# Kernel tuning notes

Hardware: AMD Instinct MI355X
Metric: run time of the kernel (lower is better)

## Reference

```python
import jax, jax.numpy as jnp
import numpy as np

B, M, L, D = 64, 128, 20, 1024


def setup_inputs() -> dict:
    key = jax.random.key(0)
    ks = jax.random.split(key, 16)
    s = 0.05  # weight scale to keep LSTM gates out of saturation
    rn = lambda k, shape: jax.random.normal(k, shape, jnp.float32) * s
    return {
        'encoder_out': jax.random.normal(ks[0], (B, M + 1, D), jnp.float32),
        'obj_seq': jax.random.randint(ks[1], (B, L), 0, M),
        'att_mask': jnp.ones((B, M + 1), jnp.int32),
        'bos_w': rn(ks[2], (1, D)),
        'eos_w': rn(ks[3], (1, D)),
        'Wp': rn(ks[4], (D, D)), 'bp': jnp.zeros((D,), jnp.float32),
        'Wih1': rn(ks[5], (4 * D, 3 * D)), 'Whh1': rn(ks[6], (4 * D, D)),
        'bih1': jnp.zeros((4 * D,), jnp.float32), 'bhh1': jnp.zeros((4 * D,), jnp.float32),
        'Wih2': rn(ks[7], (4 * D, 2 * D)), 'Whh2': rn(ks[8], (4 * D, D)),
        'bih2': jnp.zeros((4 * D,), jnp.float32), 'bhh2': jnp.zeros((4 * D,), jnp.float32),
        'Wah': rn(ks[9], (D, D)), 'bah': jnp.zeros((D,), jnp.float32),
        'wa': rn(ks[10], (D,)), 'ba': jnp.zeros((1,), jnp.float32),
        'Wae': rn(ks[11], (D, D)), 'bae': jnp.zeros((D,), jnp.float32),
        'Woe': rn(ks[12], (D, D)), 'boe': jnp.zeros((D,), jnp.float32),
    }


def _lstm_cell(x, h, c, Wih, Whh, bih, bhh):
    # torch LSTMCell gate order: i, f, g, o
    g = x @ Wih.T + bih + h @ Whh.T + bhh
    i, f, gg, o = jnp.split(g, 4, axis=-1)
    c_new = jax.nn.sigmoid(f) * c + jax.nn.sigmoid(i) * jnp.tanh(gg)
    h_new = jax.nn.sigmoid(o) * jnp.tanh(c_new)
    return h_new, c_new


def _forward(encoder_out, obj_seq, att_mask, bos_w, eos_w, Wp, bp,
             Wih1, Whh1, bih1, bhh1, Wih2, Whh2, bih2, bhh2,
             Wah, bah, wa, ba, Wae, bae, Woe, boe):
    b, _, d = encoder_out.shape
    gv = encoder_out[:, 0, :]                      # [B, D]
    att_feats = encoder_out[:, 1:, :]              # [B, M, D]
    idx = jnp.broadcast_to(obj_seq[:, :, None], obj_seq.shape + (d,)).astype(jnp.int32)
    obj_feat = jnp.take_along_axis(att_feats, idx, axis=1)          # [B, L, D]
    bos = jnp.broadcast_to(bos_w, (b, 1, d))
    obj_feat = jnp.concatenate([bos, obj_feat], axis=1)             # [B, L+1, D]
    p_att = att_feats @ Wp.T + bp                  # [B, M, D]
    amask = att_mask[:, 1:]                        # [B, M]

    def attend(h1):
        dot = jnp.tanh(p_att + (h1 @ Wah.T + bah)[:, None, :])      # [B, M, D]
        score = dot @ wa + ba[0]                                    # [B, M]
        score = jnp.where(amask == 0, -1e9, score)
        alpha = jax.nn.softmax(score, axis=-1)
        return jnp.einsum('bm,bmd->bd', alpha, att_feats)

    def step(carry, x_t):
        h1, c1, h2, c2 = carry
        inp1 = jnp.concatenate([h2, gv, x_t], axis=-1)              # [B, 3D]
        h1, c1 = _lstm_cell(inp1, h1, c1, Wih1, Whh1, bih1, bhh1)
        att = attend(h1)
        inp2 = jnp.concatenate([att, h1], axis=-1)                  # [B, 2D]
        h2, c2 = _lstm_cell(inp2, h2, c2, Wih2, Whh2, bih2, bhh2)
        return (h1, c1, h2, c2), h2

    z = jnp.zeros((b, d), encoder_out.dtype)
    _, outs = jax.lax.scan(step, (z, z, z, z), jnp.swapaxes(obj_feat, 0, 1))
    outputs = jnp.swapaxes(outs, 0, 1)             # [B, L+1, D]

    # NCE branch (cfg.LOSSES.NCE.STOP_GRAD = True)
    nce_att = jax.lax.stop_gradient(att_feats)
    afe = nce_att @ Wae.T + bae
    eos = jnp.broadcast_to(eos_w, (b, 1, d))
    afe = jnp.concatenate([eos, afe], axis=1)      # [B, M+1, D]
    ofe = outputs @ Woe.T + boe                    # [B, L+1, D]
    nce_logit = jnp.einsum('bld,bmd->blm', ofe, afe)  # [B, L+1, M+1]
    return outputs, nce_logit


def reference(encoder_out, obj_seq, att_mask, bos_w, eos_w, Wp, bp,
              Wih1, Whh1, bih1, bhh1, Wih2, Whh2, bih2, bhh2,
              Wah, bah, wa, ba, Wae, bae, Woe, boe):
    return _forward(encoder_out, obj_seq, att_mask, bos_w, eos_w, Wp, bp,
                    Wih1, Whh1, bih1, bhh1, Wih2, Whh2, bih2, bhh2,
                    Wah, bah, wa, ba, Wae, bae, Woe, boe)
```

## Files before the change

kernel.cpp:

```cpp
#include <hip/hip_runtime.h>
#include <cmath>

typedef unsigned short u16;
typedef __attribute__((ext_vector_type(8))) short short8;
typedef __attribute__((ext_vector_type(4))) float floatx4;
typedef __attribute__((address_space(3))) unsigned int lds_u32;
typedef const __attribute__((address_space(1))) unsigned int glob_u32;

__device__ __forceinline__ u16 f2bf(float f) {
    unsigned u = __float_as_uint(f);
    unsigned r = u + 0x7fffu + ((u >> 16) & 1u);
    return (u16)(r >> 16);
}
__device__ __forceinline__ float bf2f(u16 h) { return __uint_as_float(((unsigned)h) << 16); }
__device__ __forceinline__ void split2(float x, u16& hi, u16& lo) {
    hi = f2bf(x);
    lo = f2bf(x - bf2f(hi));
}
__device__ __forceinline__ float sigm(float x) {
    x = fminf(fmaxf(x, -30.f), 30.f);
    return 1.0f / (1.0f + __expf(-x));
}
__device__ __forceinline__ float ftanh(float x) {
    x = fminf(fmaxf(x, -15.f), 15.f);
    float e = __expf(2.f * x);
    return (e - 1.f) / (e + 1.f);
}
__device__ __forceinline__ void gload16(const void* g, void* l) {
    __builtin_amdgcn_global_load_lds((glob_u32*)g, (lds_u32*)l, 16, 0, 0);
}

__global__ __launch_bounds__(256) void k_cvt(const float* __restrict__ s, u16* __restrict__ d, int n4) {
    int i = blockIdx.x * 256 + threadIdx.x;
    int stride = gridDim.x * 256;
    for (; i < n4; i += stride) {
        float4 v = ((const float4*)s)[i];
        ushort4 o;
        o.x = f2bf(v.x); o.y = f2bf(v.y); o.z = f2bf(v.z); o.w = f2bf(v.w);
        ((ushort4*)d)[i] = o;
    }
}

__global__ __launch_bounds__(256) void k_cvt_att(const float* __restrict__ enc, u16* __restrict__ dst) {
    int m = blockIdx.x, b = blockIdx.y, tid = threadIdx.x;
    const float* src = enc + ((size_t)b * 129 + 1 + m) * 1024;
    float4 v = *(const float4*)(src + tid * 4);
    ushort4 o;
    o.x = f2bf(v.x); o.y = f2bf(v.y); o.z = f2bf(v.z); o.w = f2bf(v.w);
    *(ushort4*)(dst + ((size_t)b * 128 + m) * 1024 + tid * 4) = o;
}

__global__ __launch_bounds__(256) void k_splitp(const float* __restrict__ s, u16* __restrict__ hi,
                                                u16* __restrict__ lo, int n4) {
    int i = blockIdx.x * 256 + threadIdx.x;
    int stride = gridDim.x * 256;
    for (; i < n4; i += stride) {
        float4 v = ((const float4*)s)[i];
        ushort4 h, l;
        split2(v.x, h.x, l.x); split2(v.y, h.y, l.y);
        split2(v.z, h.z, l.z); split2(v.w, h.w, l.w);
        ((ushort4*)hi)[i] = h;
        ((ushort4*)lo)[i] = l;
    }
}

__global__ __launch_bounds__(256) void k_build_w1cat(const float* __restrict__ Wih1, const float* __restrict__ Whh1,
                                                     u16* __restrict__ dh, u16* __restrict__ dl) {
    int row = blockIdx.x;
    int c = threadIdx.x * 8;
    const float* src = (c < 1024) ? (Wih1 + (size_t)row * 3072 + c) : (Whh1 + (size_t)row * 1024 + (c - 1024));
    short8 h, l;
#pragma unroll
    for (int j = 0; j < 8; ++j) { u16 hh, ll; split2(src[j], hh, ll); h[j] = (short)hh; l[j] = (short)ll; }
    *(short8*)(dh + (size_t)row * 2048 + c) = h;
    *(short8*)(dl + (size_t)row * 2048 + c) = l;
}

__global__ __launch_bounds__(384) void k_build_wcat2(const float* __restrict__ Wih2, const float* __restrict__ Whh2,
                                                     u16* __restrict__ dh, u16* __restrict__ dl) {
    int row = blockIdx.x;
    int c = threadIdx.x * 8;
    const float* src = (c < 2048) ? (Wih2 + (size_t)row * 2048 + c) : (Whh2 + (size_t)row * 1024 + (c - 2048));
    short8 h, l;
#pragma unroll
    for (int j = 0; j < 8; ++j) { u16 hh, ll; split2(src[j], hh, ll); h[j] = (short)hh; l[j] = (short)ll; }
    *(short8*)(dh + (size_t)row * 3072 + c) = h;
    *(short8*)(dl + (size_t)row * 3072 + c) = l;
}

__global__ __launch_bounds__(256) void k_build_wx1(const float* __restrict__ Wih1, u16* __restrict__ dh,
                                                   u16* __restrict__ dl) {
    int row = blockIdx.x;
    int c = threadIdx.x * 8;
    const float* src = Wih1 + (size_t)row * 3072 + 1024 + c;
    short8 h, l;
#pragma unroll
    for (int j = 0; j < 8; ++j) { u16 hh, ll; split2(src[j], hh, ll); h[j] = (short)hh; l[j] = (short)ll; }
    *(short8*)(dh + (size_t)row * 2048 + c) = h;
    *(short8*)(dl + (size_t)row * 2048 + c) = l;
}

__global__ __launch_bounds__(256) void k_build_xaug(const float* __restrict__ enc, const int* __restrict__ obj,
                                                    const float* __restrict__ bos_w, u16* __restrict__ dh,
                                                    u16* __restrict__ dl) {
    int b = blockIdx.x, t = blockIdx.y, tid = threadIdx.x;
    const float* gv = enc + (size_t)b * 129 * 1024;
    const float* xr;
    if (t == 0) xr = bos_w;
    else {
        int idx = obj[b * 20 + (t - 1)];
        idx = min(max(idx, 0), 127);
        xr = enc + ((size_t)b * 129 + 1 + idx) * 1024;
    }
    size_t rowoff = ((size_t)b * 21 + t) * 2048;
    float4 v0 = *(const float4*)(gv + tid * 4);
    float4 v1 = *(const float4*)(xr + tid * 4);
    ushort4 h0, l0, h1, l1;
    split2(v0.x, h0.x, l0.x); split2(v0.y, h0.y, l0.y); split2(v0.z, h0.z, l0.z); split2(v0.w, h0.w, l0.w);
    split2(v1.x, h1.x, l1.x); split2(v1.y, h1.y, l1.y); split2(v1.z, h1.z, l1.z); split2(v1.w, h1.w, l1.w);
    *(ushort4*)(dh + rowoff + tid * 4) = h0;
    *(ushort4*)(dl + rowoff + tid * 4) = l0;
    *(ushort4*)(dh + rowoff + 1024 + tid * 4) = h1;
    *(ushort4*)(dl + rowoff + 1024 + tid * 4) = l1;
}

template <int APASS, int BPASS, int AREMAP, bool BF16OUT>
__global__ __launch_bounds__(256)
void k_gemm3(const u16* __restrict__ Ah, const u16* __restrict__ Al, int lda,
             const u16* __restrict__ Wh, const u16* __restrict__ Wl, int ldw,
             const float* __restrict__ b1, const float* __restrict__ b2,
             void* __restrict__ Cout, int ldc, int Mrows, int K) {
    constexpr int NP = APASS + BPASS;
    __shared__ char lds[2][NP][8192];
    const int tid = threadIdx.x;
    const int lane = tid & 63;
    const int lr = lane & 15, lk = lane >> 4;
    const int m0 = blockIdx.y * 128, n0 = blockIdx.x * 128;
    const int wid = tid >> 6;
    const int wr = wid >> 1, wc = wid & 1;
    const int wbyte = (tid & 192) * 16;

    floatx4 acc[4][4] = {};
    const int nt = K >> 5;

    auto stage = [&](int bb, int kt) {
        int k0 = kt * 32;
#pragma unroll
        for (int i = 0; i < 2; ++i) {
            int p = i * 256 + tid;
            int s = p ^ ((p >> 2) & 3);
            int row = s >> 2, kc = s & 3;
            size_t aoff;
            int gm = m0 + row;
            if (AREMAP == 1) aoff = (((size_t)(gm >> 7)) * 129 + 1 + (gm & 127)) * 1024 + k0 + kc * 8;
            else {
                int cm = gm < Mrows ? gm : Mrows - 1;
                aoff = (size_t)cm * lda + k0 + kc * 8;
            }
            gload16(Ah + aoff, &lds[bb][0][i * 4096 + wbyte]);
            if constexpr (APASS == 2) gload16(Al + aoff, &lds[bb][1][i * 4096 + wbyte]);
            size_t woff = (size_t)(n0 + row) * ldw + k0 + kc * 8;
            gload16(Wh + woff, &lds[bb][APASS][i * 4096 + wbyte]);
            if constexpr (BPASS == 2) gload16(Wl + woff, &lds[bb][APASS + 1][i * 4096 + wbyte]);
        }
    };

    stage(0, 0);
    __syncthreads();
    for (int t = 0; t < nt; ++t) {
        int bb = t & 1;
        if (t + 1 < nt) stage(bb ^ 1, t + 1);
        short8 ah_[4], al_[4], bh_[4], bl_[4];
#pragma unroll
        for (int mi = 0; mi < 4; ++mi) {
            int row = wr * 64 + mi * 16 + lr;
            int slot = (row * 4 + (lk ^ (row & 3))) * 16;
            ah_[mi] = *(const short8*)&lds[bb][0][slot];
            if constexpr (APASS == 2) al_[mi] = *(const short8*)&lds[bb][1][slot];
        }
#pragma unroll
        for (int ni = 0; ni < 4; ++ni) {
            int row = wc * 64 + ni * 16 + lr;
            int slot = (row * 4 + (lk ^ (row & 3))) * 16;
            bh_[ni] = *(const short8*)&lds[bb][APASS][slot];
            if constexpr (BPASS == 2) bl_[ni] = *(const short8*)&lds[bb][APASS + 1][slot];
        }
#pragma unroll
        for (int mi = 0; mi < 4; ++mi)
#pragma unroll
            for (int ni = 0; ni < 4; ++ni) {
                acc[mi][ni] = __builtin_amdgcn_mfma_f32_16x16x32_bf16(ah_[mi], bh_[ni], acc[mi][ni], 0, 0, 0);
                if constexpr (BPASS == 2)
                    acc[mi][ni] = __builtin_amdgcn_mfma_f32_16x16x32_bf16(ah_[mi], bl_[ni], acc[mi][ni], 0, 0, 0);
                if constexpr (APASS == 2)
                    acc[mi][ni] = __builtin_amdgcn_mfma_f32_16x16x32_bf16(al_[mi], bh_[ni], acc[mi][ni], 0, 0, 0);
            }
        __syncthreads();
    }
#pragma unroll
    for (int mi = 0; mi < 4; ++mi) {
#pragma unroll
        for (int r = 0; r < 4; ++r) {
            int gm = m0 + wr * 64 + mi * 16 + lk * 4 + r;
            if (AREMAP == 0 && gm >= Mrows) continue;
#pragma unroll
            for (int ni = 0; ni < 4; ++ni) {
                int gn = n0 + wc * 64 + ni * 16 + lr;
                float v = acc[mi][ni][r];
                if (b1) v += b1[gn];
                if (b2) v += b2[gn];
                if (BF16OUT) ((u16*)Cout)[(size_t)gm * ldc + gn] = f2bf(v);
                else ((float*)Cout)[(size_t)gm * ldc + gn] = v;
            }
        }
    }
}

__global__ __launch_bounds__(256)
void k_gp2(const u16* __restrict__ Xh, int ldx,
           const u16* __restrict__ Wh, const u16* __restrict__ Wl, int ldw,
           int Klen, float* __restrict__ P, int Ntot) {
    __shared__ char lds[2][8192];
    const int tid = threadIdx.x, wid = tid >> 6, lane = tid & 63;
    const int lr = lane & 15, lk = lane >> 4;
    const int n0 = blockIdx.x * 32;
    const int koff = blockIdx.y * Klen;
    floatx4 acc[2] = {};
    const int nt = Klen >> 5;

    const int sX = tid ^ ((tid >> 2) & 3);
    const size_t xoff = (size_t)(sX >> 2) * ldx + (sX & 3) * 8 + koff;
    const int xdst = (tid & 192) * 16;
    const int pw = tid & 127;
    const int sW = pw ^ ((pw >> 2) & 3);
    const size_t woff = (size_t)(n0 + (sW >> 2)) * ldw + (sW & 3) * 8 + koff;
    const u16* Wsrc = (tid < 128) ? Wh : Wl;
    const int wdst = 4096 + (wid >> 1) * 2048 + (wid & 1) * 1024;

    auto stage = [&](int bb, int kt) {
        int k0 = kt * 32;
        gload16(Xh + xoff + k0, &lds[bb][xdst]);
        gload16(Wsrc + woff + k0, &lds[bb][wdst]);
    };

    stage(0, 0);
    __syncthreads();
    for (int t = 0; t < nt; ++t) {
        int bb = t & 1;
        if (t + 1 < nt) stage(bb ^ 1, t + 1);
        int arow = wid * 16 + lr;
        short8 xh = *(const short8*)&lds[bb][(arow * 4 + (lk ^ (arow & 3))) * 16];
#pragma unroll
        for (int ni = 0; ni < 2; ++ni) {
            int r = ni * 16 + lr;
            int slot = (r * 4 + (lk ^ (r & 3))) * 16;
            short8 wh = *(const short8*)&lds[bb][4096 + slot];
            short8 wl = *(const short8*)&lds[bb][6144 + slot];
            acc[ni] = __builtin_amdgcn_mfma_f32_16x16x32_bf16(xh, wh, acc[ni], 0, 0, 0);
            acc[ni] = __builtin_amdgcn_mfma_f32_16x16x32_bf16(xh, wl, acc[ni], 0, 0, 0);
        }
        __syncthreads();
    }
    float* Pb = P + (size_t)blockIdx.y * 64 * Ntot;
#pragma unroll
    for (int ni = 0; ni < 2; ++ni)
#pragma unroll
        for (int r = 0; r < 4; ++r) {
            int b = wid * 16 + lk * 4 + r;
            Pb[(size_t)b * Ntot + n0 + ni * 16 + lr] = acc[ni][r];
        }
}

__global__ __launch_bounds__(256)
void k_finish(const float* __restrict__ P, int Ntot, int nP, const float* __restrict__ xcf,
              const float* __restrict__ b1, const float* __restrict__ b2,
              float* __restrict__ cst,
              u16* __restrict__ w1, int w1s, u16* __restrict__ w2, int w2s,
              float* __restrict__ outf, u16* __restrict__ oh) {
    int idx = blockIdx.x * 256 + threadIdx.x;
    int b = idx >> 10, d = idx & 1023;
    float g[4];
#pragma unroll
    for (int q = 0; q < 4; ++q) {
        int n = q * 1024 + d;
        float s = 0.f;
        for (int p = 0; p < nP; ++p) s += P[((size_t)p * 64 + b) * Ntot + n];
        if (xcf) s += xcf[(size_t)b * 21 * 4096 + n];
        if (b1) s += b1[n];
        if (b2) s += b2[n];
        g[q] = s;
    }
    float cp = cst[idx];
    float cn = sigm(g[1]) * cp + sigm(g[0]) * ftanh(g[2]);
    float hn = sigm(g[3]) * ftanh(cn);
    cst[idx] = cn;
    u16 hh = f2bf(hn);
    w1[b * w1s + d] = hh;
    w2[b * w2s + d] = hh;
    if (outf) outf[(size_t)b * 21 * 1024 + d] = hn;
    if (oh) oh[(size_t)b * 21 * 1024 + d] = hh;
}

__global__ __launch_bounds__(256)
void k_score(const float* __restrict__ PAH, const float* __restrict__ bah,
             const float* __restrict__ wa, const float* __restrict__ ba,
             const u16* __restrict__ Patt, const int* __restrict__ amask, float* __restrict__ SC) {
    int mc = blockIdx.x, b = blockIdx.y, tid = threadIdx.x;
    __shared__ float sah[1024], swa[1024];
    {
        int d = tid * 4;
        *(float4*)&swa[d] = *(const float4*)(wa + d);
        float4 s;
        float* sp = &s.x;
#pragma unroll
        for (int j = 0; j < 4; ++j) {
            float acc = bah[d + j];
#pragma unroll
            for (int p = 0; p < 4; ++p) acc += PAH[((size_t)p * 64 + b) * 1024 + d + j];
            sp[j] = acc;
        }
        *(float4*)&sah[d] = s;
    }
    __syncthreads();
    int wv = tid >> 6, lane = tid & 63;
    float bav = ba[0];
    for (int j = 0; j < 8; ++j) {
        int m = mc * 32 + wv * 8 + j;
        const u16* pr = Patt + ((size_t)(b * 128 + m)) * 1024;
        float part = 0.f;
#pragma unroll
        for (int c = 0; c < 4; ++c) {
            int d = c * 256 + lane * 4;
            ushort4 p4 = *(const ushort4*)(pr + d);
            float4 a4 = *(const float4*)&sah[d];
            float4 w4 = *(const float4*)&swa[d];
            part += ftanh(bf2f(p4.x) + a4.x) * w4.x + ftanh(bf2f(p4.y) + a4.y) * w4.y +
                    ftanh(bf2f(p4.z) + a4.z) * w4.z + ftanh(bf2f(p4.w) + a4.w) * w4.w;
        }
#pragma unroll
        for (int off = 32; off; off >>= 1) part += __shfl_down(part, off, 64);
        if (lane == 0) {
            float sc = part + bav;
            if (amask[b * 129 + 1 + m] == 0) sc = -1e9f;
            SC[b * 128 + m] = sc;
        }
    }
}

__global__ __launch_bounds__(256)
void k_attsum(const float* __restrict__ SC, const u16* __restrict__ attf,
              u16* __restrict__ X2h) {
    int dc = blockIdx.x, b = blockIdx.y, tid = threadIdx.x;
    __shared__ float salpha[128];
    __shared__ float sred[8];
    float sv = (tid < 128) ? SC[b * 128 + tid] : -1e30f;
    float mx = sv;
#pragma unroll
    for (int off = 32; off; off >>= 1) mx = fmaxf(mx, __shfl_down(mx, off, 64));
    if ((tid & 63) == 0) sred[tid >> 6] = mx;
    __syncthreads();
    float gmx = fmaxf(fmaxf(sred[0], sred[1]), fmaxf(sred[2], sred[3]));
    float ev = (tid < 128) ? __expf(sv - gmx) : 0.f;
    float s = ev;
#pragma unroll
    for (int off = 32; off; off >>= 1) s += __shfl_down(s, off, 64);
    if ((tid & 63) == 0) sred[4 + (tid >> 6)] = s;
    __syncthreads();
    float gsum = sred[4] + sred[5] + sred[6] + sred[7];
    if (tid < 128) salpha[tid] = ev / gsum;
    __syncthreads();
    int d = dc * 256 + tid;
    const u16* base = attf + (size_t)b * 128 * 1024 + d;
    float acc = 0.f;
#pragma unroll 8
    for (int m = 0; m < 128; ++m) acc += salpha[m] * bf2f(base[(size_t)m * 1024]);
    X2h[b * 3072 + d] = f2bf(acc);
}

__global__ __launch_bounds__(256)
void k_nce(const float* __restrict__ OFE, const float* __restrict__ AFE,
           const float* __restrict__ eos_w, float* __restrict__ nce) {
    int l = blockIdx.x, b = blockIdx.y;
    __shared__ float sofe[1024];
    int tid = threadIdx.x;
    {
        float4 v = *(const float4*)(OFE + ((size_t)b * 21 + l) * 1024 + tid * 4);
        *(float4*)&sofe[tid * 4] = v;
    }
    __syncthreads();
    int w = tid >> 6, lane = tid & 63;
    float* outp = nce + ((size_t)b * 21 + l) * 129;
    for (int j = w; j < 129; j += 4) {
        const float* ar = (j == 0) ? eos_w : AFE + ((size_t)b * 128 + (j - 1)) * 1024;
        float part = 0.f;
#pragma unroll
        for (int c = 0; c < 4; ++c) {
            float4 a4 = *(const float4*)(ar + c * 256 + lane * 4);
            float4 o4 = *(const float4*)&sofe[c * 256 + lane * 4];
            part += a4.x * o4.x + a4.y * o4.y + a4.z * o4.z + a4.w * o4.w;
        }
#pragma unroll
        for (int off = 32; off; off >>= 1) part += __shfl_down(part, off, 64);
        if (lane == 0) outp[j] = part;
    }
}

extern "C" void kernel_launch(void* const* d_in, const int* in_sizes, int n_in,
                              void* d_out, int out_size, void* d_ws, size_t ws_size,
                              hipStream_t stream) {
    const float* enc  = (const float*)d_in[0];
    const int*   obj  = (const int*)d_in[1];
    const int*   amask= (const int*)d_in[2];
    const float* bosw = (const float*)d_in[3];
    const float* eosw = (const float*)d_in[4];
    const float* Wp   = (const float*)d_in[5];
    const float* bp   = (const float*)d_in[6];
    const float* Wih1 = (const float*)d_in[7];
    const float* Whh1 = (const float*)d_in[8];
    const float* bih1 = (const float*)d_in[9];
    const float* bhh1 = (const float*)d_in[10];
    const float* Wih2 = (const float*)d_in[11];
    const float* Whh2 = (const float*)d_in[12];
    const float* bih2 = (const float*)d_in[13];
    const float* bhh2 = (const float*)d_in[14];
    const float* Wah  = (const float*)d_in[15];
    const float* bah  = (const float*)d_in[16];
    const float* wa   = (const float*)d_in[17];
    const float* ba   = (const float*)d_in[18];
    const float* Wae  = (const float*)d_in[19];
    const float* bae  = (const float*)d_in[20];
    const float* Woe  = (const float*)d_in[21];
    const float* boe  = (const float*)d_in[22];

    float* outputs = (float*)d_out;
    float* nce     = outputs + (size_t)64 * 21 * 1024;

    char* wp = (char*)d_ws;
    auto alloc = [&](size_t bytes) -> char* { char* p = wp; wp += (bytes + 255) & ~(size_t)255; return p; };
    u16* encbf  = (u16*)alloc((size_t)64 * 129 * 1024 * 2);
    u16* Wpbf   = (u16*)alloc((size_t)1024 * 1024 * 2);
    u16* Xaugh  = (u16*)alloc((size_t)1344 * 2048 * 2);
    u16* Xaugl  = (u16*)alloc((size_t)1344 * 2048 * 2);
    u16* W1h    = (u16*)alloc((size_t)4096 * 2048 * 2);
    u16* W1l    = (u16*)alloc((size_t)4096 * 2048 * 2);
    u16* W2h    = (u16*)alloc((size_t)4096 * 3072 * 2);
    u16* W2l    = (u16*)alloc((size_t)4096 * 3072 * 2);
    u16* Wahh   = (u16*)alloc((size_t)1024 * 1024 * 2);
    u16* Wahl   = (u16*)alloc((size_t)1024 * 1024 * 2);
    u16* Waeh   = (u16*)alloc((size_t)1024 * 1024 * 2);
    u16* Wael   = (u16*)alloc((size_t)1024 * 1024 * 2);
    u16* Woeh   = (u16*)alloc((size_t)1024 * 1024 * 2);
    u16* Woel   = (u16*)alloc((size_t)1024 * 1024 * 2);
    char* region1 = alloc((size_t)2 * 4096 * 2048 * 2);
    u16* Wx1h = (u16*)region1;
    u16* Wx1l = (u16*)region1 + (size_t)4096 * 2048;
    float* AFE32 = (float*)region1;
    u16* PattBf  = (u16*)alloc((size_t)8192 * 1024 * 2);
    u16* attfbf  = (u16*)alloc((size_t)64 * 128 * 1024 * 2);
    float* Xcf   = (float*)alloc((size_t)1344 * 4096 * 4);
    u16* Xouth   = (u16*)alloc((size_t)1344 * 1024 * 2);
    float* P2    = (float*)alloc((size_t)4 * 64 * 4096 * 4);
    float* OFE32 = (float*)Xaugh;
    char* sp2 = (char*)encbf;
    auto alloc2 = [&](size_t bytes) -> char* { char* p = sp2; sp2 += (bytes + 255) & ~(size_t)255; return p; };
    float* P1  = (float*)alloc2((size_t)4 * 64 * 4096 * 4);
    float* PAH = (float*)alloc2((size_t)4 * 64 * 1024 * 4);
    u16* XHh   = (u16*)alloc2((size_t)64 * 2048 * 2);
    u16* X2h   = (u16*)alloc2((size_t)64 * 3072 * 2);
    float* c1  = (float*)alloc2((size_t)64 * 1024 * 4);
    float* c2  = (float*)alloc2((size_t)64 * 1024 * 4);
    float* SC  = (float*)alloc2((size_t)64 * 128 * 4);

    dim3 blk(256);
    k_cvt<<<2048, blk, 0, stream>>>(enc, encbf, 64 * 129 * 1024 / 4);
    k_cvt_att<<<dim3(128, 64), blk, 0, stream>>>(enc, attfbf);
    k_cvt<<<1024, blk, 0, stream>>>(Wp, Wpbf, 1024 * 1024 / 4);
    k_splitp<<<1024, blk, 0, stream>>>(Wah, Wahh, Wahl, 1024 * 1024 / 4);
    k_splitp<<<1024, blk, 0, stream>>>(Wae, Waeh, Wael, 1024 * 1024 / 4);
    k_splitp<<<1024, blk, 0, stream>>>(Woe, Woeh, Woel, 1024 * 1024 / 4);
    k_build_wx1<<<4096, blk, 0, stream>>>(Wih1, Wx1h, Wx1l);
    k_build_w1cat<<<4096, blk, 0, stream>>>(Wih1, Whh1, W1h, W1l);
    k_build_wcat2<<<4096, dim3(384), 0, stream>>>(Wih2, Whh2, W2h, W2l);
    k_build_xaug<<<dim3(64, 21), blk, 0, stream>>>(enc, obj, bosw, Xaugh, Xaugl);

    k_gemm3<1, 1, 1, true><<<dim3(8, 64), blk, 0, stream>>>(
        encbf, nullptr, 0, Wpbf, nullptr, 1024, bp, nullptr, PattBf, 1024, 8192, 1024);
    k_gemm3<2, 2, 0, false><<<dim3(32, 11), blk, 0, stream>>>(
        Xaugh, Xaugl, 2048, Wx1h, Wx1l, 2048, bih1, bhh1, Xcf, 4096, 1344, 2048);
    k_gemm3<1, 2, 1, false><<<dim3(8, 64), blk, 0, stream>>>(
        encbf, nullptr, 0, Waeh, Wael, 1024, bae, nullptr, AFE32, 1024, 8192, 1024);

    hipMemsetAsync(XHh, 0, (size_t)64 * 2048 * 2, stream);
    hipMemsetAsync(X2h, 0, (size_t)64 * 3072 * 2, stream);
    hipMemsetAsync(c1, 0, (size_t)64 * 1024 * 4, stream);
    hipMemsetAsync(c2, 0, (size_t)64 * 1024 * 4, stream);

    for (int t = 0; t < 21; ++t) {
        k_gp2<<<dim3(128, 4), blk, 0, stream>>>(XHh, 2048, W1h, W1l, 2048, 512, P1, 4096);
        k_finish<<<256, blk, 0, stream>>>(P1, 4096, 4, Xcf + (size_t)t * 4096, nullptr, nullptr,
                                          c1, XHh + 1024, 2048, X2h + 1024, 3072, nullptr, nullptr);
        k_gp2<<<dim3(32, 4), blk, 0, stream>>>(XHh + 1024, 2048, Wahh, Wahl, 1024, 256, PAH, 1024);
        k_score<<<dim3(4, 64), blk, 0, stream>>>(PAH, bah, wa, ba, PattBf, amask, SC);
        k_attsum<<<dim3(4, 64), blk, 0, stream>>>(SC, attfbf, X2h);
        k_gp2<<<dim3(128, 4), blk, 0, stream>>>(X2h, 3072, W2h, W2l, 3072, 768, P2, 4096);
        k_finish<<<256, blk, 0, stream>>>(P2, 4096, 4, nullptr, bih2, bhh2,
                                          c2, XHh, 2048, X2h + 2048, 3072,
                                          outputs + (size_t)t * 1024, Xouth + (size_t)t * 1024);
    }

    k_gemm3<1, 2, 0, false><<<dim3(8, 11), blk, 0, stream>>>(
        Xouth, nullptr, 1024, Woeh, Woel, 1024, boe, nullptr, OFE32, 1024, 1344, 1024);
    k_nce<<<dim3(21, 64), blk, 0, stream>>>(OFE32, AFE32, eosw, nce);
}
```

Baseline: 1.668 ms.

## Fuse LSTM gate GEMM with cell update using gate-interleaved weights

Reorders the LSTM weight rows (and combined biases) so the four gates of each hidden unit sit next to each other. This lets a new kernel compute a 32-batch by 32-row gate tile and apply the cell update directly, without a split-K partial buffer or a separate finish kernel. The recurrent state is now kept as a bf16 hi/lo pair and uses three MFMA products, which costs extra matmul work but should improve accuracy. The fused kernel runs the full K per block on only 256 blocks, giving up the split-K parallelism of the old path.

```diff
diff --git a/kernel.cpp b/kernel.cpp
--- a/kernel.cpp
+++ b/kernel.cpp
@@ -64,40 +64,50 @@
     }
 }
 
-__global__ __launch_bounds__(256) void k_build_w1cat(const float* __restrict__ Wih1, const float* __restrict__ Whh1,
-                                                     u16* __restrict__ dh, u16* __restrict__ dl) {
-    int row = blockIdx.x;
+__global__ __launch_bounds__(256) void k_build_w1cat_i(const float* __restrict__ Wih1, const float* __restrict__ Whh1,
+                                                       u16* __restrict__ dh, u16* __restrict__ dl) {
+    int r = blockIdx.x;
+    int srcrow = (r & 3) * 1024 + (r >> 2);
     int c = threadIdx.x * 8;
-    const float* src = (c < 1024) ? (Wih1 + (size_t)row * 3072 + c) : (Whh1 + (size_t)row * 1024 + (c - 1024));
+    const float* src = (c < 1024) ? (Wih1 + (size_t)srcrow * 3072 + c) : (Whh1 + (size_t)srcrow * 1024 + (c - 1024));
     short8 h, l;
 #pragma unroll
     for (int j = 0; j < 8; ++j) { u16 hh, ll; split2(src[j], hh, ll); h[j] = (short)hh; l[j] = (short)ll; }
-    *(short8*)(dh + (size_t)row * 2048 + c) = h;
-    *(short8*)(dl + (size_t)row * 2048 + c) = l;
-}
-
-__global__ __launch_bounds__(384) void k_build_wcat2(const float* __restrict__ Wih2, const float* __restrict__ Whh2,
-                                                     u16* __restrict__ dh, u16* __restrict__ dl) {
-    int row = blockIdx.x;
+    *(short8*)(dh + (size_t)r * 2048 + c) = h;
+    *(short8*)(dl + (size_t)r * 2048 + c) = l;
+}
+
+__global__ __launch_bounds__(384) void k_build_wcat2_i(const float* __restrict__ Wih2, const float* __restrict__ Whh2,
+                                                       u16* __restrict__ dh, u16* __restrict__ dl) {
+    int r = blockIdx.x;
+    int srcrow = (r & 3) * 1024 + (r >> 2);
     int c = threadIdx.x * 8;
-    const float* src = (c < 2048) ? (Wih2 + (size_t)row * 2048 + c) : (Whh2 + (size_t)row * 1024 + (c - 2048));
+    const float* src = (c < 2048) ? (Wih2 + (size_t)srcrow * 2048 + c) : (Whh2 + (size_t)srcrow * 1024 + (c - 2048));
     short8 h, l;
 #pragma unroll
     for (int j = 0; j < 8; ++j) { u16 hh, ll; split2(src[j], hh, ll); h[j] = (short)hh; l[j] = (short)ll; }
-    *(short8*)(dh + (size_t)row * 3072 + c) = h;
-    *(short8*)(dl + (size_t)row * 3072 + c) = l;
-}
-
-__global__ __launch_bounds__(256) void k_build_wx1(const float* __restrict__ Wih1, u16* __restrict__ dh,
-                                                   u16* __restrict__ dl) {
-    int row = blockIdx.x;
+    *(short8*)(dh + (size_t)r * 3072 + c) = h;
+    *(short8*)(dl + (size_t)r * 3072 + c) = l;
+}
+
+__global__ __launch_bounds__(256) void k_build_wx1_i(const float* __restrict__ Wih1, u16* __restrict__ dh,
+                                                     u16* __restrict__ dl) {
+    int r = blockIdx.x;
+    int srcrow = (r & 3) * 1024 + (r >> 2);
     int c = threadIdx.x * 8;
-    const float* src = Wih1 + (size_t)row * 3072 + 1024 + c;
+    const float* src = Wih1 + (size_t)srcrow * 3072 + 1024 + c;
     short8 h, l;
 #pragma unroll
     for (int j = 0; j < 8; ++j) { u16 hh, ll; split2(src[j], hh, ll); h[j] = (short)hh; l[j] = (short)ll; }
-    *(short8*)(dh + (size_t)row * 2048 + c) = h;
-    *(short8*)(dl + (size_t)row * 2048 + c) = l;
+    *(short8*)(dh + (size_t)r * 2048 + c) = h;
+    *(short8*)(dl + (size_t)r * 2048 + c) = l;
+}
+
+__global__ __launch_bounds__(256) void k_mkbias(const float* __restrict__ s1, const float* __restrict__ s2,
+                                                float* __restrict__ dst) {
+    int r = blockIdx.x * 256 + threadIdx.x;
+    int srcn = (r & 3) * 1024 + (r >> 2);
+    dst[r] = s1[srcn] + s2[srcn];
 }
 
 __global__ __launch_bounds__(256) void k_build_xaug(const float* __restrict__ enc, const int* __restrict__ obj,
@@ -216,6 +226,107 @@
     }
 }
 
+template <int KK>
+__global__ __launch_bounds__(256)
+void k_cell3(const u16* __restrict__ Xh_, const u16* __restrict__ Xl_, int ldx,
+             const u16* __restrict__ Wh, const u16* __restrict__ Wl,
+             const float* __restrict__ addf, int add_bstride,
+             const float* __restrict__ bias,
+             float* __restrict__ cst,
+             u16* __restrict__ w1h, u16* __restrict__ w1l, int w1s,
+             u16* __restrict__ w2h, u16* __restrict__ w2l, int w2s,
+             float* __restrict__ outf, u16* __restrict__ oh) {
+    __shared__ __align__(16) char smem[2][8192];
+    const int tid = threadIdx.x, wid = tid >> 6, lane = tid & 63;
+    const int lr = lane & 15, lk = lane >> 4;
+    const int bg = blockIdx.x >> 7, dg = blockIdx.x & 127;
+    const int b0 = bg * 32, r0 = dg * 32;
+    const int s = lane ^ ((lane >> 2) & 3);
+    const int srow = s >> 2, sc8 = (s & 3) * 8;
+
+    floatx4 acc[2][2] = {};
+    constexpr int nt = KK / 32;
+
+    auto stage = [&](int bb, int kt) {
+        int k0 = kt * 32;
+        char* buf = smem[bb];
+        if (wid == 0) {
+            gload16(Xh_ + (size_t)(b0 + srow) * ldx + k0 + sc8, buf + 0);
+            gload16(Xl_ + (size_t)(b0 + srow) * ldx + k0 + sc8, buf + 2048);
+        } else if (wid == 1) {
+            gload16(Xh_ + (size_t)(b0 + 16 + srow) * ldx + k0 + sc8, buf + 1024);
+            gload16(Xl_ + (size_t)(b0 + 16 + srow) * ldx + k0 + sc8, buf + 3072);
+        } else if (wid == 2) {
+            gload16(Wh + (size_t)(r0 + srow) * KK + k0 + sc8, buf + 4096);
+            gload16(Wl + (size_t)(r0 + srow) * KK + k0 + sc8, buf + 6144);
+        } else {
+            gload16(Wh + (size_t)(r0 + 16 + srow) * KK + k0 + sc8, buf + 5120);
+            gload16(Wl + (size_t)(r0 + 16 + srow) * KK + k0 + sc8, buf + 7168);
+        }
+    };
+
+    stage(0, 0);
+    __syncthreads();
+    for (int t = 0; t < nt; ++t) {
+        int bb = t & 1;
+        if (t + 1 < nt) stage(bb ^ 1, t + 1);
+        const char* buf = smem[bb];
+        int off = (lr * 4 + (lk ^ (lr & 3))) * 16;
+        short8 xh[2], xl[2], wh[2], wl[2];
+#pragma unroll
+        for (int i = 0; i < 2; ++i) {
+            xh[i] = *(const short8*)(buf + i * 1024 + off);
+            xl[i] = *(const short8*)(buf + 2048 + i * 1024 + off);
+            wh[i] = *(const short8*)(buf + 4096 + i * 1024 + off);
+            wl[i] = *(const short8*)(buf + 6144 + i * 1024 + off);
+        }
+#pragma unroll
+        for (int mi = 0; mi < 2; ++mi)
+#pragma unroll
+            for (int ni = 0; ni < 2; ++ni) {
+                acc[mi][ni] = __builtin_amdgcn_mfma_f32_16x16x32_bf16(xh[mi], wh[ni], acc[mi][ni], 0, 0, 0);
+                acc[mi][ni] = __builtin_amdgcn_mfma_f32_16x16x32_bf16(xh[mi], wl[ni], acc[mi][ni], 0, 0, 0);
+                acc[mi][ni] = __builtin_amdgcn_mfma_f32_16x16x32_bf16(xl[mi], wh[ni], acc[mi][ni], 0, 0, 0);
+            }
+        __syncthreads();
+    }
+    float* Gs = (float*)smem;
+#pragma unroll
+    for (int mi = 0; mi < 2; ++mi)
+#pragma unroll
+        for (int ni = 0; ni < 2; ++ni)
+#pragma unroll
+            for (int j = 0; j < 4; ++j)
+                Gs[(mi * 16 + lk * 4 + j) * 36 + ni * 16 + lr] = acc[mi][ni][j];
+    __syncthreads();
+    {
+        int bl_ = tid >> 3;
+        int dl = tid & 7;
+        int b = b0 + bl_;
+        int d = dg * 8 + dl;
+        float4 g = *(const float4*)&Gs[bl_ * 36 + dl * 4];
+        if (addf) {
+            float4 av = *(const float4*)(addf + (size_t)b * add_bstride + dg * 32 + dl * 4);
+            g.x += av.x; g.y += av.y; g.z += av.z; g.w += av.w;
+        }
+        if (bias) {
+            float4 bv = *(const float4*)(bias + dg * 32 + dl * 4);
+            g.x += bv.x; g.y += bv.y; g.z += bv.z; g.w += bv.w;
+        }
+        int ci = b * 1024 + d;
+        float cp = cst[ci];
+        float cn = sigm(g.y) * cp + sigm(g.x) * ftanh(g.z);
+        float hn = sigm(g.w) * ftanh(cn);
+        cst[ci] = cn;
+        u16 hh, hl;
+        split2(hn, hh, hl);
+        w1h[b * w1s + d] = hh; w1l[b * w1s + d] = hl;
+        w2h[b * w2s + d] = hh; w2l[b * w2s + d] = hl;
+        if (outf) outf[(size_t)b * 21 * 1024 + d] = hn;
+        if (oh) oh[(size_t)b * 21 * 1024 + d] = hh;
+    }
+}
+
 __global__ __launch_bounds__(256)
 void k_gp2(const u16* __restrict__ Xh, int ldx,
            const u16* __restrict__ Wh, const u16* __restrict__ Wl, int ldw,
@@ -272,36 +383,6 @@
 }
 
 __global__ __launch_bounds__(256)
-void k_finish(const float* __restrict__ P, int Ntot, int nP, const float* __restrict__ xcf,
-              const float* __restrict__ b1, const float* __restrict__ b2,
-              float* __restrict__ cst,
-              u16* __restrict__ w1, int w1s, u16* __restrict__ w2, int w2s,
-              float* __restrict__ outf, u16* __restrict__ oh) {
-    int idx = blockIdx.x * 256 + threadIdx.x;
-    int b = idx >> 10, d = idx & 1023;
-    float g[4];
-#pragma unroll
-    for (int q = 0; q < 4; ++q) {
-        int n = q * 1024 + d;
-        float s = 0.f;
-        for (int p = 0; p < nP; ++p) s += P[((size_t)p * 64 + b) * Ntot + n];
-        if (xcf) s += xcf[(size_t)b * 21 * 4096 + n];
-        if (b1) s += b1[n];
-        if (b2) s += b2[n];
-        g[q] = s;
-    }
-    float cp = cst[idx];
-    float cn = sigm(g[1]) * cp + sigm(g[0]) * ftanh(g[2]);
-    float hn = sigm(g[3]) * ftanh(cn);
-    cst[idx] = cn;
-    u16 hh = f2bf(hn);
-    w1[b * w1s + d] = hh;
-    w2[b * w2s + d] = hh;
-    if (outf) outf[(size_t)b * 21 * 1024 + d] = hn;
-    if (oh) oh[(size_t)b * 21 * 1024 + d] = hh;
-}
-
-__global__ __launch_bounds__(256)
 void k_score(const float* __restrict__ PAH, const float* __restrict__ bah,
              const float* __restrict__ wa, const float* __restrict__ ba,
              const u16* __restrict__ Patt, const int* __restrict__ amask, float* __restrict__ SC) {
@@ -349,7 +430,7 @@
 
 __global__ __launch_bounds__(256)
 void k_attsum(const float* __restrict__ SC, const u16* __restrict__ attf,
-              u16* __restrict__ X2h) {
+              u16* __restrict__ X2h, u16* __restrict__ X2l) {
     int dc = blockIdx.x, b = blockIdx.y, tid = threadIdx.x;
     __shared__ float salpha[128];
     __shared__ float sred[8];
@@ -374,7 +455,10 @@
     float acc = 0.f;
 #pragma unroll 8
     for (int m = 0; m < 128; ++m) acc += salpha[m] * bf2f(base[(size_t)m * 1024]);
-    X2h[b * 3072 + d] = f2bf(acc);
+    u16 hh, hl;
+    split2(acc, hh, hl);
+    X2h[b * 3072 + d] = hh;
+    X2l[b * 3072 + d] = hl;
 }
 
 __global__ __launch_bounds__(256)
@@ -451,6 +535,8 @@
     u16* Wael   = (u16*)alloc((size_t)1024 * 1024 * 2);
     u16* Woeh   = (u16*)alloc((size_t)1024 * 1024 * 2);
     u16* Woel   = (u16*)alloc((size_t)1024 * 1024 * 2);
+    float* bias1i = (float*)alloc(4096 * 4);
+    float* bias2i = (float*)alloc(4096 * 4);
     char* region1 = alloc((size_t)2 * 4096 * 2048 * 2);
     u16* Wx1h = (u16*)region1;
     u16* Wx1l = (u16*)region1 + (size_t)4096 * 2048;
@@ -459,14 +545,14 @@
     u16* attfbf  = (u16*)alloc((size_t)64 * 128 * 1024 * 2);
     float* Xcf   = (float*)alloc((size_t)1344 * 4096 * 4);
     u16* Xouth   = (u16*)alloc((size_t)1344 * 1024 * 2);
-    float* P2    = (float*)alloc((size_t)4 * 64 * 4096 * 4);
     float* OFE32 = (float*)Xaugh;
     char* sp2 = (char*)encbf;
     auto alloc2 = [&](size_t bytes) -> char* { char* p = sp2; sp2 += (bytes + 255) & ~(size_t)255; return p; };
-    float* P1  = (float*)alloc2((size_t)4 * 64 * 4096 * 4);
     float* PAH = (float*)alloc2((size_t)4 * 64 * 1024 * 4);
     u16* XHh   = (u16*)alloc2((size_t)64 * 2048 * 2);
+    u16* XHl   = (u16*)alloc2((size_t)64 * 2048 * 2);
     u16* X2h   = (u16*)alloc2((size_t)64 * 3072 * 2);
+    u16* X2l   = (u16*)alloc2((size_t)64 * 3072 * 2);
     float* c1  = (float*)alloc2((size_t)64 * 1024 * 4);
     float* c2  = (float*)alloc2((size_t)64 * 1024 * 4);
     float* SC  = (float*)alloc2((size_t)64 * 128 * 4);
@@ -478,34 +564,38 @@
     k_splitp<<<1024, blk, 0, stream>>>(Wah, Wahh, Wahl, 1024 * 1024 / 4);
     k_splitp<<<1024, blk, 0, stream>>>(Wae, Waeh, Wael, 1024 * 1024 / 4);
     k_splitp<<<1024, blk, 0, stream>>>(Woe, Woeh, Woel, 1024 * 1024 / 4);
-    k_build_wx1<<<4096, blk, 0, stream>>>(Wih1, Wx1h, Wx1l);
-    k_build_w1cat<<<4096, blk, 0, stream>>>(Wih1, Whh1, W1h, W1l);
-    k_build_wcat2<<<4096, dim3(384), 0, stream>>>(Wih2, Whh2, W2h, W2l);
+    k_build_wx1_i<<<4096, blk, 0, stream>>>(Wih1, Wx1h, Wx1l);
+    k_build_w1cat_i<<<4096, blk, 0, stream>>>(Wih1, Whh1, W1h, W1l);
+    k_build_wcat2_i<<<4096, dim3(384), 0, stream>>>(Wih2, Whh2, W2h, W2l);
+    k_mkbias<<<16, blk, 0, stream>>>(bih1, bhh1, bias1i);
+    k_mkbias<<<16, blk, 0, stream>>>(bih2, bhh2, bias2i);
     k_build_xaug<<<dim3(64, 21), blk, 0, stream>>>(enc, obj, bosw, Xaugh, Xaugl);
 
     k_gemm3<1, 1, 1, true><<<dim3(8, 64), blk, 0, stream>>>(
         encbf, nullptr, 0, Wpbf, nullptr, 1024, bp, nullptr, PattBf, 1024, 8192, 1024);
     k_gemm3<2, 2, 0, false><<<dim3(32, 11), blk, 0, stream>>>(
-        Xaugh, Xaugl, 2048, Wx1h, Wx1l, 2048, bih1, bhh1, Xcf, 4096, 1344, 2048);
+        Xaugh, Xaugl, 2048, Wx1h, Wx1l, 2048, bias1i, nullptr, Xcf, 4096, 1344, 2048);
     k_gemm3<1, 2, 1, false><<<dim3(8, 64), blk, 0, stream>>>(
         encbf, nullptr, 0, Waeh, Wael, 1024, bae, nullptr, AFE32, 1024, 8192, 1024);
 
     hipMemsetAsync(XHh, 0, (size_t)64 * 2048 * 2, stream);
+    hipMemsetAsync(XHl, 0, (size_t)64 * 2048 * 2, stream);
     hipMemsetAsync(X2h, 0, (size_t)64 * 3072 * 2, stream);
+    hipMemsetAsync(X2l, 0, (size_t)64 * 3072 * 2, stream);
     hipMemsetAsync(c1, 0, (size_t)64 * 1024 * 4, stream);
     hipMemsetAsync(c2, 0, (size_t)64 * 1024 * 4, stream);
 
     for (int t = 0; t < 21; ++t) {
-        k_gp2<<<dim3(128, 4), blk, 0, stream>>>(XHh, 2048, W1h, W1l, 2048, 512, P1, 4096);
-        k_finish<<<256, blk, 0, stream>>>(P1, 4096, 4, Xcf + (size_t)t * 4096, nullptr, nullptr,
-                                          c1, XHh + 1024, 2048, X2h + 1024, 3072, nullptr, nullptr);
+        k_cell3<2048><<<256, blk, 0, stream>>>(
+            XHh, XHl, 2048, W1h, W1l, Xcf + (size_t)t * 4096, 21 * 4096, nullptr,
+            c1, XHh + 1024, XHl + 1024, 2048, X2h + 1024, X2l + 1024, 3072, nullptr, nullptr);
         k_gp2<<<dim3(32, 4), blk, 0, stream>>>(XHh + 1024, 2048, Wahh, Wahl, 1024, 256, PAH, 1024);
         k_score<<<dim3(4, 64), blk, 0, stream>>>(PAH, bah, wa, ba, PattBf, amask, SC);
-        k_attsum<<<dim3(4, 64), blk, 0, stream>>>(SC, attfbf, X2h);
-        k_gp2<<<dim3(128, 4), blk, 0, stream>>>(X2h, 3072, W2h, W2l, 3072, 768, P2, 4096);
-        k_finish<<<256, blk, 0, stream>>>(P2, 4096, 4, nullptr, bih2, bhh2,
-                                          c2, XHh, 2048, X2h + 2048, 3072,
-                                          outputs + (size_t)t * 1024, Xouth + (size_t)t * 1024);
+        k_attsum<<<dim3(4, 64), blk, 0, stream>>>(SC, attfbf, X2h, X2l);
+        k_cell3<3072><<<256, blk, 0, stream>>>(
+            X2h, X2l, 3072, W2h, W2l, nullptr, 0, bias2i,
+            c2, XHh, XHl, 2048, X2h + 2048, X2l + 2048, 3072,
+            outputs + (size_t)t * 1024, Xouth + (size_t)t * 1024);
     }
 
     k_gemm3<1, 2, 0, false><<<dim3(8, 11), blk, 0, stream>>>(
```

Measured after the change: 2.423 ms. 1.45x slower.

## Fuse attention score and softmax-sum kernels; store NCE projections in bf16

Applied to the files above, without the earlier changes.

Merges the per-step attention scoring and softmax-weighted sum into one kernel per batch row, keeping scores in shared memory and dropping one launch per timestep (21 total). Separately, the AFE and OFE projection outputs are written as bf16 instead of fp32, halving traffic in the NCE dot-product kernel. The fused kernel uses only 64 blocks instead of 256+256, so per-step parallelism drops and each block serially scores 128 rows. The bf16 storage also lowers NCE logit precision.

```diff
diff --git a/kernel.cpp b/kernel.cpp
--- a/kernel.cpp
+++ b/kernel.cpp
@@ -302,11 +302,16 @@
 }
 
 __global__ __launch_bounds__(256)
-void k_score(const float* __restrict__ PAH, const float* __restrict__ bah,
-             const float* __restrict__ wa, const float* __restrict__ ba,
-             const u16* __restrict__ Patt, const int* __restrict__ amask, float* __restrict__ SC) {
-    int mc = blockIdx.x, b = blockIdx.y, tid = threadIdx.x;
+void k_att(const float* __restrict__ PAH, const float* __restrict__ bah,
+           const float* __restrict__ wa, const float* __restrict__ ba,
+           const u16* __restrict__ Patt, const int* __restrict__ amask,
+           const u16* __restrict__ attf, u16* __restrict__ X2att) {
+    int b = blockIdx.x, tid = threadIdx.x;
     __shared__ float sah[1024], swa[1024];
+    __shared__ float sSC[128];
+    __shared__ float sred[8];
+    int wv = tid >> 6, lane = tid & 63;
+
     {
         int d = tid * 4;
         *(float4*)&swa[d] = *(const float4*)(wa + d);
@@ -322,10 +327,10 @@
         *(float4*)&sah[d] = s;
     }
     __syncthreads();
-    int wv = tid >> 6, lane = tid & 63;
+
     float bav = ba[0];
-    for (int j = 0; j < 8; ++j) {
-        int m = mc * 32 + wv * 8 + j;
+    for (int j = 0; j < 32; ++j) {
+        int m = wv * 32 + j;
         const u16* pr = Patt + ((size_t)(b * 128 + m)) * 1024;
         float part = 0.f;
 #pragma unroll
@@ -342,62 +347,75 @@
         if (lane == 0) {
             float sc = part + bav;
             if (amask[b * 129 + 1 + m] == 0) sc = -1e9f;
-            SC[b * 128 + m] = sc;
-        }
-    }
-}
-
-__global__ __launch_bounds__(256)
-void k_attsum(const float* __restrict__ SC, const u16* __restrict__ attf,
-              u16* __restrict__ X2h) {
-    int dc = blockIdx.x, b = blockIdx.y, tid = threadIdx.x;
-    __shared__ float salpha[128];
-    __shared__ float sred[8];
-    float sv = (tid < 128) ? SC[b * 128 + tid] : -1e30f;
+            sSC[m] = sc;
+        }
+    }
+    __syncthreads();
+
+    float sv = (tid < 128) ? sSC[tid] : -1e30f;
     float mx = sv;
 #pragma unroll
     for (int off = 32; off; off >>= 1) mx = fmaxf(mx, __shfl_down(mx, off, 64));
-    if ((tid & 63) == 0) sred[tid >> 6] = mx;
+    if (lane == 0) sred[wv] = mx;
     __syncthreads();
     float gmx = fmaxf(fmaxf(sred[0], sred[1]), fmaxf(sred[2], sred[3]));
     float ev = (tid < 128) ? __expf(sv - gmx) : 0.f;
     float s = ev;
 #pragma unroll
     for (int off = 32; off; off >>= 1) s += __shfl_down(s, off, 64);
-    if ((tid & 63) == 0) sred[4 + (tid >> 6)] = s;
+    if (lane == 0) sred[4 + wv] = s;
     __syncthreads();
     float gsum = sred[4] + sred[5] + sred[6] + sred[7];
-    if (tid < 128) salpha[tid] = ev / gsum;
-    __syncthreads();
-    int d = dc * 256 + tid;
-    const u16* base = attf + (size_t)b * 128 * 1024 + d;
-    float acc = 0.f;
-#pragma unroll 8
-    for (int m = 0; m < 128; ++m) acc += salpha[m] * bf2f(base[(size_t)m * 1024]);
-    X2h[b * 3072 + d] = f2bf(acc);
+    if (tid < 128) sSC[tid] = ev / gsum;
+    __syncthreads();
+
+    {
+        int d = tid * 4;
+        const u16* base = attf + (size_t)b * 128 * 1024 + d;
+        float4 acc = make_float4(0.f, 0.f, 0.f, 0.f);
+#pragma unroll 4
+        for (int m = 0; m < 128; ++m) {
+            float al = sSC[m];
+            ushort4 v = *(const ushort4*)(base + (size_t)m * 1024);
+            acc.x += al * bf2f(v.x); acc.y += al * bf2f(v.y);
+            acc.z += al * bf2f(v.z); acc.w += al * bf2f(v.w);
+        }
+        ushort4 o;
+        o.x = f2bf(acc.x); o.y = f2bf(acc.y); o.z = f2bf(acc.z); o.w = f2bf(acc.w);
+        *(ushort4*)(X2att + (size_t)b * 3072 + d) = o;
+    }
 }
 
 __global__ __launch_bounds__(256)
-void k_nce(const float* __restrict__ OFE, const float* __restrict__ AFE,
-           const float* __restrict__ eos_w, float* __restrict__ nce) {
+void k_nce_bf(const u16* __restrict__ OFE, const u16* __restrict__ AFE,
+              const float* __restrict__ eos_w, float* __restrict__ nce) {
     int l = blockIdx.x, b = blockIdx.y;
-    __shared__ float sofe[1024];
+    __shared__ u16 sofe[1024];
     int tid = threadIdx.x;
-    {
-        float4 v = *(const float4*)(OFE + ((size_t)b * 21 + l) * 1024 + tid * 4);
-        *(float4*)&sofe[tid * 4] = v;
-    }
+    *(ushort4*)&sofe[tid * 4] = *(const ushort4*)(OFE + ((size_t)b * 21 + l) * 1024 + tid * 4);
     __syncthreads();
     int w = tid >> 6, lane = tid & 63;
     float* outp = nce + ((size_t)b * 21 + l) * 129;
     for (int j = w; j < 129; j += 4) {
-        const float* ar = (j == 0) ? eos_w : AFE + ((size_t)b * 128 + (j - 1)) * 1024;
         float part = 0.f;
-#pragma unroll
-        for (int c = 0; c < 4; ++c) {
-            float4 a4 = *(const float4*)(ar + c * 256 + lane * 4);
-            float4 o4 = *(const float4*)&sofe[c * 256 + lane * 4];
-            part += a4.x * o4.x + a4.y * o4.y + a4.z * o4.z + a4.w * o4.w;
+        if (j == 0) {
+#pragma unroll
+            for (int c = 0; c < 4; ++c) {
+                int d = c * 256 + lane * 4;
+                float4 a4 = *(const float4*)(eos_w + d);
+                ushort4 o4 = *(const ushort4*)&sofe[d];
+                part += a4.x * bf2f(o4.x) + a4.y * bf2f(o4.y) + a4.z * bf2f(o4.z) + a4.w * bf2f(o4.w);
+            }
+        } else {
+            const u16* ar = AFE + ((size_t)b * 128 + (j - 1)) * 1024;
+#pragma unroll
+            for (int c = 0; c < 4; ++c) {
+                int d = c * 256 + lane * 4;
+                ushort4 a4 = *(const ushort4*)(ar + d);
+                ushort4 o4 = *(const ushort4*)&sofe[d];
+                part += bf2f(a4.x) * bf2f(o4.x) + bf2f(a4.y) * bf2f(o4.y) +
+                        bf2f(a4.z) * bf2f(o4.z) + bf2f(a4.w) * bf2f(o4.w);
+            }
         }
 #pragma unroll
         for (int off = 32; off; off >>= 1) part += __shfl_down(part, off, 64);
@@ -454,13 +472,13 @@
     char* region1 = alloc((size_t)2 * 4096 * 2048 * 2);
     u16* Wx1h = (u16*)region1;
     u16* Wx1l = (u16*)region1 + (size_t)4096 * 2048;
-    float* AFE32 = (float*)region1;
+    u16* AFEbf = (u16*)region1;
     u16* PattBf  = (u16*)alloc((size_t)8192 * 1024 * 2);
     u16* attfbf  = (u16*)alloc((size_t)64 * 128 * 1024 * 2);
     float* Xcf   = (float*)alloc((size_t)1344 * 4096 * 4);
     u16* Xouth   = (u16*)alloc((size_t)1344 * 1024 * 2);
     float* P2    = (float*)alloc((size_t)4 * 64 * 4096 * 4);
-    float* OFE32 = (float*)Xaugh;
+    u16* OFEbf = Xaugh;
     char* sp2 = (char*)encbf;
     auto alloc2 = [&](size_t bytes) -> char* { char* p = sp2; sp2 += (bytes + 255) & ~(size_t)255; return p; };
     float* P1  = (float*)alloc2((size_t)4 * 64 * 4096 * 4);
@@ -469,7 +487,6 @@
     u16* X2h   = (u16*)alloc2((size_t)64 * 3072 * 2);
     float* c1  = (float*)alloc2((size_t)64 * 1024 * 4);
     float* c2  = (float*)alloc2((size_t)64 * 1024 * 4);
-    float* SC  = (float*)alloc2((size_t)64 * 128 * 4);
 
     dim3 blk(256);
     k_cvt<<<2048, blk, 0, stream>>>(enc, encbf, 64 * 129 * 1024 / 4);
@@ -487,8 +504,8 @@
         encbf, nullptr, 0, Wpbf, nullptr, 1024, bp, nullptr, PattBf, 1024, 8192, 1024);
     k_gemm3<2, 2, 0, false><<<dim3(32, 11), blk, 0, stream>>>(
         Xaugh, Xaugl, 2048, Wx1h, Wx1l, 2048, bih1, bhh1, Xcf, 4096, 1344, 2048);
-    k_gemm3<1, 2, 1, false><<<dim3(8, 64), blk, 0, stream>>>(
-        encbf, nullptr, 0, Waeh, Wael, 1024, bae, nullptr, AFE32, 1024, 8192, 1024);
+    k_gemm3<1, 2, 1, true><<<dim3(8, 64), blk, 0, stream>>>(
+        encbf, nullptr, 0, Waeh, Wael, 1024, bae, nullptr, AFEbf, 1024, 8192, 1024);
 
     hipMemsetAsync(XHh, 0, (size_t)64 * 2048 * 2, stream);
     hipMemsetAsync(X2h, 0, (size_t)64 * 3072 * 2, stream);
@@ -500,15 +517,14 @@
         k_finish<<<256, blk, 0, stream>>>(P1, 4096, 4, Xcf + (size_t)t * 4096, nullptr, nullptr,
                                           c1, XHh + 1024, 2048, X2h + 1024, 3072, nullptr, nullptr);
         k_gp2<<<dim3(32, 4), blk, 0, stream>>>(XHh + 1024, 2048, Wahh, Wahl, 1024, 256, PAH, 1024);
-        k_score<<<dim3(4, 64), blk, 0, stream>>>(PAH, bah, wa, ba, PattBf, amask, SC);
-        k_attsum<<<dim3(4, 64), blk, 0, stream>>>(SC, attfbf, X2h);
+        k_att<<<64, blk, 0, stream>>>(PAH, bah, wa, ba, PattBf, amask, attfbf, X2h);
         k_gp2<<<dim3(128, 4), blk, 0, stream>>>(X2h, 3072, W2h, W2l, 3072, 768, P2, 4096);
         k_finish<<<256, blk, 0, stream>>>(P2, 4096, 4, nullptr, bih2, bhh2,
                                           c2, XHh, 2048, X2h + 2048, 3072,
                                           outputs + (size_t)t * 1024, Xouth + (size_t)t * 1024);
     }
 
-    k_gemm3<1, 2, 0, false><<<dim3(8, 11), blk, 0, stream>>>(
-        Xouth, nullptr, 1024, Woeh, Woel, 1024, boe, nullptr, OFE32, 1024, 1344, 1024);
-    k_nce<<<dim3(21, 64), blk, 0, stream>>>(OFE32, AFE32, eosw, nce);
-}
+    k_gemm3<1, 2, 0, true><<<dim3(8, 11), blk, 0, stream>>>(
+        Xouth, nullptr, 1024, Woeh, Woel, 1024, boe, nullptr, OFEbf, 1024, 1344, 1024);
+    k_nce_bf<<<dim3(21, 64), blk, 0, stream>>>(OFEbf, AFEbf, eosw, nce);
+}
```

Result: slower. 2.240 ms (+34.3%).
